# Kernel optimization log

Hardware: AMD Instinct MI355X
Metric: run time of the kernel (lower is better)

The kernel has to match this reference:

```python
import jax, jax.numpy as jnp
import numpy as np

B, N, G = 32, 1024, 8   # batch, Nvecs (= k_in), Nglobals
K_OUT, H = 128, 128     # MLP output width, hidden width
D_IN = 1 + N + G        # MLP input width: [u, norm, dots]


def setup_inputs() -> dict:
    key = jax.random.key(0)
    ks = jax.random.split(key, 8)
    x = jax.random.uniform(ks[0], (B, N, 3), dtype=jnp.float32)  # positive coords -> dots >= 0
    u = jax.random.normal(ks[1], (B, G), dtype=jnp.float32)
    s0 = 1.0 / np.sqrt(D_IN)
    s1 = 1.0 / np.sqrt(H)
    W0 = jax.random.normal(ks[2], (D_IN, H), dtype=jnp.float32) * s0
    b0 = jnp.zeros((H,), dtype=jnp.float32)
    W1 = jax.random.normal(ks[3], (H, H), dtype=jnp.float32) * s1
    b1 = jnp.zeros((H,), dtype=jnp.float32)
    W2 = jax.random.normal(ks[4], (H, K_OUT), dtype=jnp.float32) * s1
    b2 = jnp.zeros((K_OUT,), dtype=jnp.float32)
    return {"x": x, "u": u, "W0": W0, "b0": b0, "W1": W1, "b1": b1, "W2": W2, "b2": b2}


def reference(x, u, W0, b0, W1, b1, W2, b2):
    # x: [B, N, 3], u: [B, G]
    norms = jnp.linalg.norm(x, axis=-1, keepdims=True)            # [B, N, 1]
    dots = jnp.sqrt(jnp.einsum('bid,bjd->bij', x, x))             # [B, N, N]
    u_rep = jnp.broadcast_to(u[:, None, :], (x.shape[0], x.shape[1], u.shape[-1]))
    scalars = jnp.concatenate([u_rep, norms, dots], axis=-1)      # [B, N, G+1+N]
    # MLP (Linear -> LeakyReLU -> Linear -> LeakyReLU -> Linear)
    h = jax.nn.leaky_relu(scalars @ W0 + b0)
    h = jax.nn.leaky_relu(h @ W1 + b1)
    fk = h @ W2 + b2                                              # [B, N, K_OUT]
    # outer product 'bio,bid->biod' followed by mean over i == fused contraction
    out = jnp.einsum('bio,bid->bod', fk, x) / x.shape[1]          # [B, K_OUT, 3]
    return out
```

## Files before the change

### kernel.cpp

```cpp
#include <hip/hip_runtime.h>
#include <hip/hip_fp16.h>

typedef _Float16 f16;
typedef f16 f16x4 __attribute__((ext_vector_type(4)));
typedef f16 f16x8 __attribute__((ext_vector_type(8)));
typedef float f32x4 __attribute__((ext_vector_type(4)));

#define NN 1024

#define WT0_OFF   0
#define WT1_OFF   262144
#define WT2_OFF   294912
#define W8_OFF    327680
#define BIAS0_OFF 328192

__global__ __launch_bounds__(256) void prep_kernel(
    const float* __restrict__ u,  const float* __restrict__ W0,
    const float* __restrict__ b0, const float* __restrict__ W1,
    const float* __restrict__ W2,
    f16* __restrict__ Wt0, f16* __restrict__ Wt1, f16* __restrict__ Wt2,
    float* __restrict__ w8v, float* __restrict__ bias0)
{
    __shared__ __align__(16) f16 T[128 * 130];
    const int t = threadIdx.x;
    const int blk = blockIdx.x;
    if (blk < 16) {
        const int j0 = blk * 64;
        for (int k = 0; k < 32; ++k) {
            int flat = k * 256 + t;
            int j = flat >> 7, h = flat & 127;
            T[j * 130 + h] = (f16)W0[(9 + j0 + j) * 128 + h];
        }
        __syncthreads();
        for (int k = 0; k < 32; ++k) {
            int flat = k * 256 + t;
            int h = flat >> 6, jj = flat & 63;
            Wt0[h * 1024 + j0 + jj] = T[jj * 130 + h];
        }
    } else if (blk < 18) {
        const float* Ws = (blk == 16) ? W1 : W2;
        f16* Wd = (blk == 16) ? Wt1 : Wt2;
        for (int k = 0; k < 64; ++k) {
            int flat = k * 256 + t;
            int hi = flat >> 7, ho = flat & 127;
            T[ho * 130 + hi] = (f16)Ws[hi * 128 + ho];
        }
        __syncthreads();
        for (int k = 0; k < 64; ++k) {
            int flat = k * 256 + t;
            int ho = flat >> 7, hi = flat & 127;
            Wd[ho * 128 + hi] = T[ho * 130 + hi];
        }
    } else {
        if (t < 128) w8v[t] = W0[8 * 128 + t];
        for (int k = 0; k < 16; ++k) {
            int flat = k * 256 + t;
            int b = flat >> 7, h = flat & 127;
            float s = b0[h];
#pragma unroll
            for (int g = 0; g < 8; ++g) s += u[b * 8 + g] * W0[g * 128 + h];
            bias0[b * 128 + h] = s;
        }
    }
}

__global__ __launch_bounds__(256, 2) void fused_kernel(
    const float* __restrict__ x,   const float* __restrict__ b1p,
    const float* __restrict__ b2p,
    const f16* __restrict__ Wt0, const f16* __restrict__ Wt1,
    const f16* __restrict__ Wt2, const float* __restrict__ w8v,
    const float* __restrict__ bias0, float* __restrict__ outp)
{
    __shared__ __align__(16) f16 Dsh[2][64 * 64];
    __shared__ __align__(16) f16 Wsh[2][128 * 64];
    __shared__ __align__(16) float xi[64 * 4];
    __shared__ float normv[64];
    __shared__ float biass[128];
    __shared__ float w8s[128];

    const int t = threadIdx.x;
    const int b = blockIdx.x >> 4;
    const int i0 = (blockIdx.x & 15) * 64;

    if (t < 192) {
        int i = t / 3, d = t - i * 3;
        xi[i * 4 + d] = x[(size_t)(b * NN + i0 + i) * 3 + d];
    }
    if (t < 128) { biass[t] = bias0[b * 128 + t]; w8s[t] = w8v[t]; }
    __syncthreads();
    if (t < 64) {
        float a0 = xi[t * 4], a1 = xi[t * 4 + 1], a2 = xi[t * 4 + 2];
        normv[t] = __builtin_amdgcn_sqrtf(a0 * a0 + a1 * a1 + a2 * a2);
        xi[t * 4 + 3] = 0.f;
    }
    __syncthreads();

    const int lane = t & 63, wv = t >> 6;
    const int wm = wv >> 1, wn = wv & 1;
    const int lm = lane & 15, q = lane >> 4;

    f16x4 bi[4];
#pragma unroll
    for (int it = 0; it < 4; ++it) {
        f16x4 v; v[0] = (f16)0; v[1] = (f16)0; v[2] = (f16)0; v[3] = (f16)0;
        if (q == 0) {
            int ii = it * 16 + lm;
            v[0] = (f16)xi[ii * 4];
            v[1] = (f16)xi[ii * 4 + 1];
            v[2] = (f16)xi[ii * 4 + 2];
        }
        bi[it] = v;
    }

    f32x4 acc[2][4];
    auto zero_acc = [&]() {
#pragma unroll
        for (int mt = 0; mt < 2; ++mt)
#pragma unroll
            for (int nt = 0; nt < 4; ++nt)
#pragma unroll
                for (int e = 0; e < 4; ++e) acc[mt][nt][e] = 0.f;
    };
    zero_acc();

    auto load_aj = [&](int jc) -> f16x4 {
        f16x4 a; a[0] = (f16)0; a[1] = (f16)0; a[2] = (f16)0; a[3] = (f16)0;
        if (q == 0) {
            const float* p = x + (size_t)(b * NN + jc * 64 + wv * 16 + lm) * 3;
            a[0] = (f16)p[0]; a[1] = (f16)p[1]; a[2] = (f16)p[2];
        }
        return a;
    };

    auto dotstore = [&](f16x4 aj, int buf) {
        f32x4 cg[4];
#pragma unroll
        for (int it = 0; it < 4; ++it) {
            f32x4 z; z[0] = 0.f; z[1] = 0.f; z[2] = 0.f; z[3] = 0.f;
            cg[it] = __builtin_amdgcn_mfma_f32_16x16x16f16(aj, bi[it], z, 0, 0, 0);
        }
#pragma unroll
        for (int it = 0; it < 4; ++it) {
            f16x4 dv;
#pragma unroll
            for (int r = 0; r < 4; ++r)
                dv[r] = (f16)__builtin_amdgcn_sqrtf(fmaxf(cg[it][r], 0.f));
            int row = it * 16 + lm;
            int colstart = wv * 16 + q * 4;
            int addr = row * 64 + (((colstart & ~7) ^ ((row & 7) << 3)) | (colstart & 7));
            *(f16x4*)&Dsh[buf][addr] = dv;
        }
    };

    auto mfma2 = [&](const f16* Ab, const f16* Bb) {
#pragma unroll
        for (int ks = 0; ks < 2; ++ks) {
            const int col = ks * 32 + q * 8;
            f16x8 af[2], bf[4];
#pragma unroll
            for (int mt = 0; mt < 2; ++mt) {
                int row = wm * 32 + mt * 16 + lm;
                af[mt] = *(const f16x8*)(Ab + row * 64 + (col ^ ((row & 7) << 3)));
            }
#pragma unroll
            for (int nt = 0; nt < 4; ++nt) {
                int row = wn * 64 + nt * 16 + lm;
                bf[nt] = *(const f16x8*)(Bb + row * 64 + (col ^ ((row & 7) << 3)));
            }
#pragma unroll
            for (int mt = 0; mt < 2; ++mt)
#pragma unroll
                for (int nt = 0; nt < 4; ++nt)
                    acc[mt][nt] = __builtin_amdgcn_mfma_f32_16x16x32_f16(
                        af[mt], bf[nt], acc[mt][nt], 0, 0, 0);
        }
    };

    auto stageW = [&](const f16* src, int stride, int srcCol, int buf) {
#pragma unroll
        for (int k = 0; k < 4; ++k) {
            int uu = t + k * 256;
            int row = uu >> 3, unit = uu & 7;
            uint4 v = *(const uint4*)(src + row * stride + srcCol + unit * 8);
            int addr = row * 64 + ((unit * 8) ^ ((row & 7) << 3));
            *(uint4*)&Wsh[buf][addr] = v;
        }
    };

    dotstore(load_aj(0), 0);
    stageW(Wt0, 1024, 0, 0);
    __syncthreads();

    int cur = 0;
    for (int jc = 0; jc < 16; ++jc) {
        const int nxt = cur ^ 1;
        const f16* wsrc = (jc < 15) ? Wt0 : Wt1;
        const int wstride = (jc < 15) ? 1024 : 128;
        const int wcol = (jc < 15) ? (jc + 1) * 64 : 0;
        uint4 wreg[4];
#pragma unroll
        for (int k = 0; k < 4; ++k) {
            int uu = t + k * 256;
            int row = uu >> 3, unit = uu & 7;
            wreg[k] = *(const uint4*)(wsrc + row * wstride + wcol + unit * 8);
        }
        if (jc < 15) dotstore(load_aj(jc + 1), nxt);
#pragma unroll
        for (int k = 0; k < 4; ++k) {
            int uu = t + k * 256;
            int row = uu >> 3, unit = uu & 7;
            int addr = row * 64 + ((unit * 8) ^ ((row & 7) << 3));
            *(uint4*)&Wsh[nxt][addr] = wreg[k];
        }
        mfma2(Dsh[cur], Wsh[cur]);
        __syncthreads();
        cur = nxt;
    }

#pragma unroll
    for (int mt = 0; mt < 2; ++mt)
#pragma unroll
        for (int nt = 0; nt < 4; ++nt) {
            const int h = wn * 64 + nt * 16 + lm;
            const float bh = biass[h], w8h = w8s[h];
            const int hh = h & 63;
#pragma unroll
            for (int r = 0; r < 4; ++r) {
                int i = wm * 32 + mt * 16 + q * 4 + r;
                float val = acc[mt][nt][r] + bh + normv[i] * w8h;
                val = val > 0.f ? val : 0.01f * val;
                int addr = i * 64 + (((hh & ~7) ^ ((i & 7) << 3)) | (hh & 7));
                Dsh[wn][addr] = (f16)val;
            }
        }
    stageW(Wt1, 128, 64, 1);
    __syncthreads();

    zero_acc();
    mfma2(Dsh[0], Wsh[0]);
    mfma2(Dsh[1], Wsh[1]);
    __syncthreads();

#pragma unroll
    for (int mt = 0; mt < 2; ++mt)
#pragma unroll
        for (int nt = 0; nt < 4; ++nt) {
            const int h = wn * 64 + nt * 16 + lm;
            const float bh = b1p[h];
            const int hh = h & 63;
#pragma unroll
            for (int r = 0; r < 4; ++r) {
                int i = wm * 32 + mt * 16 + q * 4 + r;
                float val = acc[mt][nt][r] + bh;
                val = val > 0.f ? val : 0.01f * val;
                int addr = i * 64 + (((hh & ~7) ^ ((i & 7) << 3)) | (hh & 7));
                Dsh[wn][addr] = (f16)val;
            }
        }
    stageW(Wt2, 128, 0, 0);
    stageW(Wt2, 128, 64, 1);
    __syncthreads();

    zero_acc();
    mfma2(Dsh[0], Wsh[0]);
    mfma2(Dsh[1], Wsh[1]);

    float p[4][3];
#pragma unroll
    for (int nt = 0; nt < 4; ++nt)
#pragma unroll
        for (int d = 0; d < 3; ++d) p[nt][d] = 0.f;
    float bo[4];
#pragma unroll
    for (int nt = 0; nt < 4; ++nt) bo[nt] = b2p[wn * 64 + nt * 16 + lm];
#pragma unroll
    for (int mt = 0; mt < 2; ++mt)
#pragma unroll
        for (int r = 0; r < 4; ++r) {
            int i = wm * 32 + mt * 16 + q * 4 + r;
            float x0 = xi[i * 4], x1 = xi[i * 4 + 1], x2 = xi[i * 4 + 2];
#pragma unroll
            for (int nt = 0; nt < 4; ++nt) {
                float fkv = acc[mt][nt][r] + bo[nt];
                p[nt][0] = fmaf(fkv, x0, p[nt][0]);
                p[nt][1] = fmaf(fkv, x1, p[nt][1]);
                p[nt][2] = fmaf(fkv, x2, p[nt][2]);
            }
        }
#pragma unroll
    for (int nt = 0; nt < 4; ++nt)
#pragma unroll
        for (int d = 0; d < 3; ++d) {
            float s = p[nt][d];
            s += __shfl_xor(s, 16);
            s += __shfl_xor(s, 32);
            if (q == 0) {
                int o = wn * 64 + nt * 16 + lm;
                atomicAdd(&outp[(b * 128 + o) * 3 + d], s * (1.0f / 1024.0f));
            }
        }
}

extern "C" void kernel_launch(void* const* d_in, const int* in_sizes, int n_in,
                              void* d_out, int out_size, void* d_ws, size_t ws_size,
                              hipStream_t stream) {
    const float* x  = (const float*)d_in[0];
    const float* u  = (const float*)d_in[1];
    const float* W0 = (const float*)d_in[2];
    const float* b0 = (const float*)d_in[3];
    const float* W1 = (const float*)d_in[4];
    const float* b1 = (const float*)d_in[5];
    const float* W2 = (const float*)d_in[6];
    const float* b2 = (const float*)d_in[7];

    char* ws = (char*)d_ws;
    f16*   Wt0   = (f16*)(ws + WT0_OFF);
    f16*   Wt1   = (f16*)(ws + WT1_OFF);
    f16*   Wt2   = (f16*)(ws + WT2_OFF);
    float* w8v   = (float*)(ws + W8_OFF);
    float* bias0 = (float*)(ws + BIAS0_OFF);
    float* out   = (float*)d_out;

    hipMemsetAsync(d_out, 0, (size_t)out_size * sizeof(float), stream);
    prep_kernel<<<19, 256, 0, stream>>>(u, W0, b0, W1, W2, Wt0, Wt1, Wt2, w8v, bias0);
    fused_kernel<<<512, 256, 0, stream>>>(x, b1, b2, Wt0, Wt1, Wt2, w8v, bias0, out);
}
```

Measured before the change: 100.4 us.

## Pre-swizzle weight image and stage chunks via direct global-to-LDS loads

The prep kernel now writes all weights into one pre-swizzled fp16 image of 20 contiguous 64-column chunks, spread over many more blocks, and also zeroes the output so the separate memset disappears. The fused kernel stages each chunk straight into LDS with global_load_lds instead of going through registers. It also preloads all 16 x fragments up front, fully unrolls the main loop and raises the occupancy hint to 3. This targets register-staged copy overhead, launch count and the serial prep latency, at the cost of more registers for the aj array. In the last loop iteration stage(16) reads chunk 16, which is W1's first half as the next layer needs, so the logic is consistent.

```diff
diff --git a/kernel.cpp b/kernel.cpp
--- a/kernel.cpp
+++ b/kernel.cpp
@@ -8,9 +8,7 @@
 
 #define NN 1024
 
-#define WT0_OFF   0
-#define WT1_OFF   262144
-#define WT2_OFF   294912
+#define IMG_OFF   0
 #define W8_OFF    327680
 #define BIAS0_OFF 328192
 
@@ -18,58 +16,51 @@
     const float* __restrict__ u,  const float* __restrict__ W0,
     const float* __restrict__ b0, const float* __restrict__ W1,
     const float* __restrict__ W2,
-    f16* __restrict__ Wt0, f16* __restrict__ Wt1, f16* __restrict__ Wt2,
-    float* __restrict__ w8v, float* __restrict__ bias0)
+    f16* __restrict__ img, float* __restrict__ w8v, float* __restrict__ bias0,
+    float* __restrict__ outp)
 {
-    __shared__ __align__(16) f16 T[128 * 130];
     const int t = threadIdx.x;
     const int blk = blockIdx.x;
-    if (blk < 16) {
-        const int j0 = blk * 64;
-        for (int k = 0; k < 32; ++k) {
-            int flat = k * 256 + t;
-            int j = flat >> 7, h = flat & 127;
-            T[j * 130 + h] = (f16)W0[(9 + j0 + j) * 128 + h];
-        }
-        __syncthreads();
-        for (int k = 0; k < 32; ++k) {
-            int flat = k * 256 + t;
-            int h = flat >> 6, jj = flat & 63;
-            Wt0[h * 1024 + j0 + jj] = T[jj * 130 + h];
-        }
-    } else if (blk < 18) {
-        const float* Ws = (blk == 16) ? W1 : W2;
-        f16* Wd = (blk == 16) ? Wt1 : Wt2;
-        for (int k = 0; k < 64; ++k) {
-            int flat = k * 256 + t;
-            int hi = flat >> 7, ho = flat & 127;
-            T[ho * 130 + hi] = (f16)Ws[hi * 128 + ho];
-        }
-        __syncthreads();
-        for (int k = 0; k < 64; ++k) {
-            int flat = k * 256 + t;
-            int ho = flat >> 7, hi = flat & 127;
-            Wd[ho * 128 + hi] = T[ho * 130 + hi];
-        }
+    if (blk < 160) {
+        int flat = blk * 1024 + t * 4;
+        int c = flat >> 13;
+        int rem = flat & 8191;
+        int r = rem >> 6;
+        int s = rem & 63;
+        int colb = s ^ ((r & 7) << 3);
+        f16x4 v;
+#pragma unroll
+        for (int e = 0; e < 4; ++e) {
+            int col = colb + e;
+            float val;
+            if (c < 16)       val = W0[(9 + c * 64 + col) * 128 + r];
+            else if (c == 16) val = W1[col * 128 + r];
+            else if (c == 17) val = W1[(64 + col) * 128 + r];
+            else if (c == 18) val = W2[col * 128 + r];
+            else              val = W2[(64 + col) * 128 + r];
+            v[e] = (f16)val;
+        }
+        *(f16x4*)&img[flat] = v;
+    } else if (blk < 176) {
+        int idx = (blk - 160) * 256 + t;
+        int b = idx >> 7, h = idx & 127;
+        float s = b0[h];
+#pragma unroll
+        for (int g = 0; g < 8; ++g) s += u[b * 8 + g] * W0[g * 128 + h];
+        bias0[idx] = s;
+    } else if (blk == 176) {
+        if (t < 128) w8v[t] = W0[8 * 128 + t];
     } else {
-        if (t < 128) w8v[t] = W0[8 * 128 + t];
-        for (int k = 0; k < 16; ++k) {
-            int flat = k * 256 + t;
-            int b = flat >> 7, h = flat & 127;
-            float s = b0[h];
-#pragma unroll
-            for (int g = 0; g < 8; ++g) s += u[b * 8 + g] * W0[g * 128 + h];
-            bias0[b * 128 + h] = s;
-        }
+        int idx = (blk - 177) * 1024 + t * 4;
+        if (idx < 12288) { float4 z = {0.f, 0.f, 0.f, 0.f}; *(float4*)&outp[idx] = z; }
     }
 }
 
-__global__ __launch_bounds__(256, 2) void fused_kernel(
-    const float* __restrict__ x,   const float* __restrict__ b1p,
-    const float* __restrict__ b2p,
-    const f16* __restrict__ Wt0, const f16* __restrict__ Wt1,
-    const f16* __restrict__ Wt2, const float* __restrict__ w8v,
-    const float* __restrict__ bias0, float* __restrict__ outp)
+__global__ __launch_bounds__(256, 3) void fused_kernel(
+    const float* __restrict__ x, const float* __restrict__ b1p,
+    const float* __restrict__ b2p, const f16* __restrict__ img,
+    const float* __restrict__ w8v, const float* __restrict__ bias0,
+    float* __restrict__ outp)
 {
     __shared__ __align__(16) f16 Dsh[2][64 * 64];
     __shared__ __align__(16) f16 Wsh[2][128 * 64];
@@ -91,9 +82,7 @@
     if (t < 64) {
         float a0 = xi[t * 4], a1 = xi[t * 4 + 1], a2 = xi[t * 4 + 2];
         normv[t] = __builtin_amdgcn_sqrtf(a0 * a0 + a1 * a1 + a2 * a2);
-        xi[t * 4 + 3] = 0.f;
-    }
-    __syncthreads();
+    }
 
     const int lane = t & 63, wv = t >> 6;
     const int wm = wv >> 1, wn = wv & 1;
@@ -112,32 +101,46 @@
         bi[it] = v;
     }
 
-    f32x4 acc[2][4];
-    auto zero_acc = [&]() {
-#pragma unroll
-        for (int mt = 0; mt < 2; ++mt)
-#pragma unroll
-            for (int nt = 0; nt < 4; ++nt)
-#pragma unroll
-                for (int e = 0; e < 4; ++e) acc[mt][nt][e] = 0.f;
-    };
-    zero_acc();
-
-    auto load_aj = [&](int jc) -> f16x4 {
+    f16x4 aj[16];
+#pragma unroll
+    for (int jc = 0; jc < 16; ++jc) {
         f16x4 a; a[0] = (f16)0; a[1] = (f16)0; a[2] = (f16)0; a[3] = (f16)0;
         if (q == 0) {
             const float* p = x + (size_t)(b * NN + jc * 64 + wv * 16 + lm) * 3;
             a[0] = (f16)p[0]; a[1] = (f16)p[1]; a[2] = (f16)p[2];
         }
-        return a;
-    };
-
-    auto dotstore = [&](f16x4 aj, int buf) {
+        aj[jc] = a;
+    }
+
+    f32x4 acc[2][4];
+    auto zero_acc = [&]() {
+#pragma unroll
+        for (int mt = 0; mt < 2; ++mt)
+#pragma unroll
+            for (int nt = 0; nt < 4; ++nt)
+#pragma unroll
+                for (int e = 0; e < 4; ++e) acc[mt][nt][e] = 0.f;
+    };
+    zero_acc();
+
+    auto stage = [&](int c, int buf) {
+        const f16* g = img + c * 8192;
+#pragma unroll
+        for (int k = 0; k < 4; ++k) {
+            int off = (t + k * 256) * 8;
+            __builtin_amdgcn_global_load_lds(
+                (const __attribute__((address_space(1))) unsigned int*)(g + off),
+                (__attribute__((address_space(3))) unsigned int*)(&Wsh[buf][off]),
+                16, 0, 0);
+        }
+    };
+
+    auto dotstore = [&](f16x4 ajf, int buf) {
         f32x4 cg[4];
 #pragma unroll
         for (int it = 0; it < 4; ++it) {
             f32x4 z; z[0] = 0.f; z[1] = 0.f; z[2] = 0.f; z[3] = 0.f;
-            cg[it] = __builtin_amdgcn_mfma_f32_16x16x16f16(aj, bi[it], z, 0, 0, 0);
+            cg[it] = __builtin_amdgcn_mfma_f32_16x16x16f16(ajf, bi[it], z, 0, 0, 0);
         }
 #pragma unroll
         for (int it = 0; it < 4; ++it) {
@@ -176,45 +179,17 @@
         }
     };
 
-    auto stageW = [&](const f16* src, int stride, int srcCol, int buf) {
-#pragma unroll
-        for (int k = 0; k < 4; ++k) {
-            int uu = t + k * 256;
-            int row = uu >> 3, unit = uu & 7;
-            uint4 v = *(const uint4*)(src + row * stride + srcCol + unit * 8);
-            int addr = row * 64 + ((unit * 8) ^ ((row & 7) << 3));
-            *(uint4*)&Wsh[buf][addr] = v;
-        }
-    };
-
-    dotstore(load_aj(0), 0);
-    stageW(Wt0, 1024, 0, 0);
-    __syncthreads();
-
-    int cur = 0;
+    stage(0, 0);
+    dotstore(aj[0], 0);
+    __syncthreads();
+
+#pragma unroll
     for (int jc = 0; jc < 16; ++jc) {
-        const int nxt = cur ^ 1;
-        const f16* wsrc = (jc < 15) ? Wt0 : Wt1;
-        const int wstride = (jc < 15) ? 1024 : 128;
-        const int wcol = (jc < 15) ? (jc + 1) * 64 : 0;
-        uint4 wreg[4];
-#pragma unroll
-        for (int k = 0; k < 4; ++k) {
-            int uu = t + k * 256;
-            int row = uu >> 3, unit = uu & 7;
-            wreg[k] = *(const uint4*)(wsrc + row * wstride + wcol + unit * 8);
-        }
-        if (jc < 15) dotstore(load_aj(jc + 1), nxt);
-#pragma unroll
-        for (int k = 0; k < 4; ++k) {
-            int uu = t + k * 256;
-            int row = uu >> 3, unit = uu & 7;
-            int addr = row * 64 + ((unit * 8) ^ ((row & 7) << 3));
-            *(uint4*)&Wsh[nxt][addr] = wreg[k];
-        }
+        const int cur = jc & 1, nxt = cur ^ 1;
+        stage(jc + 1, nxt);
+        if (jc < 15) dotstore(aj[jc + 1], nxt);
         mfma2(Dsh[cur], Wsh[cur]);
         __syncthreads();
-        cur = nxt;
     }
 
 #pragma unroll
@@ -233,7 +208,7 @@
                 Dsh[wn][addr] = (f16)val;
             }
         }
-    stageW(Wt1, 128, 64, 1);
+    stage(17, 1);
     __syncthreads();
 
     zero_acc();
@@ -257,8 +232,8 @@
                 Dsh[wn][addr] = (f16)val;
             }
         }
-    stageW(Wt2, 128, 0, 0);
-    stageW(Wt2, 128, 64, 1);
+    stage(18, 0);
+    stage(19, 1);
     __syncthreads();
 
     zero_acc();
@@ -314,14 +289,11 @@
     const float* b2 = (const float*)d_in[7];
 
     char* ws = (char*)d_ws;
-    f16*   Wt0   = (f16*)(ws + WT0_OFF);
-    f16*   Wt1   = (f16*)(ws + WT1_OFF);
-    f16*   Wt2   = (f16*)(ws + WT2_OFF);
+    f16*   img   = (f16*)(ws + IMG_OFF);
     float* w8v   = (float*)(ws + W8_OFF);
     float* bias0 = (float*)(ws + BIAS0_OFF);
     float* out   = (float*)d_out;
 
-    hipMemsetAsync(d_out, 0, (size_t)out_size * sizeof(float), stream);
-    prep_kernel<<<19, 256, 0, stream>>>(u, W0, b0, W1, W2, Wt0, Wt1, Wt2, w8v, bias0);
-    fused_kernel<<<512, 256, 0, stream>>>(x, b1, b2, Wt0, Wt1, Wt2, w8v, bias0, out);
+    prep_kernel<<<189, 256, 0, stream>>>(u, W0, b0, W1, W2, img, w8v, bias0, out);
+    fused_kernel<<<512, 256, 0, stream>>>(x, b1, b2, img, w8v, bias0, out);
 }
```

New measurement: 96.45 us. -4.0%, faster.
